# Performance work log

Measured on AMD Instinct MI355X. Metric: run time of the kernel, lower is better.

Reference implementation:

```python
import jax, jax.numpy as jnp
import numpy as np

D = 1024      # model_dim (input_dim)
H = 2048      # hidden_size_per_expert (hardcoded in module)
E = 8         # num_experts
K = 2         # topk
T = 8192      # tokens (batch after view)


def setup_inputs() -> dict:
    key = jax.random.key(0)
    ks = jax.random.split(key, 6)
    s_in = 1.0 / np.sqrt(D)
    s_h = 1.0 / np.sqrt(H)
    return {
        "x": jax.random.normal(ks[0], (T, D), dtype=jnp.float32),
        "wg": jax.random.normal(ks[1], (D, E), dtype=jnp.float32) * s_in,   # gate Linear(D,E,bias=False)
        "w1": jax.random.normal(ks[2], (E, D, H), dtype=jnp.float32) * s_in,
        "b1": jnp.zeros((E, H), dtype=jnp.float32),
        "w2": jax.random.normal(ks[3], (E, H, D), dtype=jnp.float32) * s_h,
        "b2": jnp.zeros((E, D), dtype=jnp.float32),
    }


def _moe(x, wg, w1, b1, w2, b2):
    # top-k gating (Tutel 'top' gate, k=K)
    logits = x @ wg                         # [T,E]
    scores = jax.nn.softmax(logits, -1)     # [T,E]
    topv, topi = jax.lax.top_k(scores, K)   # [T,K]
    sel = jax.nn.one_hot(topi, E, dtype=x.dtype)          # [T,K,E]
    combine = jnp.einsum('tk,tke->te', topv, sel)          # sparse combine weights [T,E]
    # GShard-style load-balance aux loss (top-1 dispatch mask)
    ce = sel[:, 0, :].mean(0)               # fraction of tokens whose top1 is e
    me = scores.mean(0)                     # mean gate prob per expert
    l_aux = jnp.sum(me * ce) * E
    # expert FFN (dense over experts; combine zeros out non-selected)
    h = jax.nn.relu(jnp.einsum('td,edh->teh', x, w1) + b1)  # [T,E,H]
    y = jnp.einsum('teh,ehd->ted', h, w2) + b2              # [T,E,D]
    out = jnp.einsum('te,ted->td', combine, y)              # [T,D]
    return out, l_aux


def reference(x, wg, w1, b1, w2, b2):
    return _moe(x, wg, w1, b1, w2, b2)
```

## Files before the change

### kernel.cpp

```cpp
#include <hip/hip_runtime.h>
#include <stdint.h>

#define T_TOK 8192
#define DIM   1024
#define HID   2048
#define NE    8

#define BM 128
#define BN 128
#define BK 64

#define GB_TOK 32

typedef float floatx4 __attribute__((ext_vector_type(4)));
typedef short shortx8 __attribute__((ext_vector_type(8)));

typedef __attribute__((address_space(3))) void       lds_void;
typedef const __attribute__((address_space(1))) void gbl_void;

__device__ __forceinline__ unsigned short f2bf(float f) {
  unsigned int u = __float_as_uint(f);
  unsigned int r = 0x7fffu + ((u >> 16) & 1u);
  return (unsigned short)((u + r) >> 16);
}

__global__ __launch_bounds__(256) void cast_x_kernel(const float* __restrict__ x,
                                                     unsigned short* __restrict__ xb) {
  size_t i = ((size_t)blockIdx.x * 256 + threadIdx.x) * 4;
  float4 v = *reinterpret_cast<const float4*>(x + i);
  ushort4 o;
  o.x = f2bf(v.x); o.y = f2bf(v.y); o.z = f2bf(v.z); o.w = f2bf(v.w);
  *reinterpret_cast<ushort4*>(xb + i) = o;
}

__global__ __launch_bounds__(256) void transpose_cast_kernel(const float* __restrict__ in,
                                                             unsigned short* __restrict__ out,
                                                             int R, int C) {
  __shared__ float tile[32][33];
  const size_t eoff = (size_t)blockIdx.z * R * C;
  const float* ip = in + eoff;
  unsigned short* op = out + eoff;
  int c0 = blockIdx.x * 32, r0 = blockIdx.y * 32;
  int tx = threadIdx.x, ty = threadIdx.y;
#pragma unroll
  for (int i = 0; i < 4; i++)
    tile[ty + i * 8][tx] = ip[(size_t)(r0 + ty + i * 8) * C + (c0 + tx)];
  __syncthreads();
#pragma unroll
  for (int i = 0; i < 4; i++)
    op[(size_t)(c0 + ty + i * 8) * R + (r0 + tx)] = f2bf(tile[tx][ty + i * 8]);
}

__global__ __launch_bounds__(256) void gate_kernel(const float* __restrict__ x,
                                                   const float* __restrict__ wg,
                                                   int* counts, int* top1cnt, float* ssum,
                                                   int* tok_list, float* wgt_list) {
  __shared__ int   lds_cnt[8];
  __shared__ int   lds_top1[8];
  __shared__ float lds_ssum[4][8];
  __shared__ int   tk_e[GB_TOK][2];
  __shared__ int   tk_r[GB_TOK][2];
  __shared__ float tk_w[GB_TOK][2];
  __shared__ int   base[8];

  const int tid = threadIdx.x;
  const int wave = tid >> 6;
  const int lane = tid & 63;

  if (tid < 8) { lds_cnt[tid] = 0; lds_top1[tid] = 0; }
  if (tid < 32) lds_ssum[tid >> 3][tid & 7] = 0.f;
  __syncthreads();

  float ssum_local[8];
#pragma unroll
  for (int e = 0; e < 8; e++) ssum_local[e] = 0.f;

  for (int it = 0; it < GB_TOK / 4; it++) {
    const int lt = it * 4 + wave;
    const int t = blockIdx.x * GB_TOK + lt;

    float acc[8];
#pragma unroll
    for (int e = 0; e < 8; e++) acc[e] = 0.f;
    const float* xr = x + (size_t)t * DIM;
#pragma unroll
    for (int i = 0; i < 16; i++) {
      int d = i * 64 + lane;
      float xv = xr[d];
      const float4* wr = reinterpret_cast<const float4*>(wg + d * 8);
      float4 w0 = wr[0], w1 = wr[1];
      acc[0] += xv * w0.x; acc[1] += xv * w0.y; acc[2] += xv * w0.z; acc[3] += xv * w0.w;
      acc[4] += xv * w1.x; acc[5] += xv * w1.y; acc[6] += xv * w1.z; acc[7] += xv * w1.w;
    }
#pragma unroll
    for (int e = 0; e < 8; e++) {
#pragma unroll
      for (int off = 32; off > 0; off >>= 1) acc[e] += __shfl_xor(acc[e], off, 64);
    }
    if (lane == 0) {
      float mx = acc[0];
#pragma unroll
      for (int e = 1; e < 8; e++) mx = fmaxf(mx, acc[e]);
      float s[8], sum = 0.f;
#pragma unroll
      for (int e = 0; e < 8; e++) { s[e] = expf(acc[e] - mx); sum += s[e]; }
      float inv = 1.f / sum;
#pragma unroll
      for (int e = 0; e < 8; e++) { s[e] *= inv; ssum_local[e] += s[e]; }
      int i1 = 0;
#pragma unroll
      for (int e = 1; e < 8; e++) if (s[e] > s[i1]) i1 = e;
      int i2 = (i1 == 0) ? 1 : 0;
#pragma unroll
      for (int e = 0; e < 8; e++) if (e != i1 && s[e] > s[i2]) i2 = e;
      atomicAdd(&lds_top1[i1], 1);
      int r1 = atomicAdd(&lds_cnt[i1], 1);
      int r2 = atomicAdd(&lds_cnt[i2], 1);
      tk_e[lt][0] = i1; tk_r[lt][0] = r1; tk_w[lt][0] = s[i1];
      tk_e[lt][1] = i2; tk_r[lt][1] = r2; tk_w[lt][1] = s[i2];
    }
  }
  if (lane == 0) {
#pragma unroll
    for (int e = 0; e < 8; e++) lds_ssum[wave][e] = ssum_local[e];
  }
  __syncthreads();
  if (tid < 8) {
    base[tid] = atomicAdd(&counts[tid], lds_cnt[tid]);
    atomicAdd(&top1cnt[tid], lds_top1[tid]);
    atomicAdd(&ssum[tid],
              lds_ssum[0][tid] + lds_ssum[1][tid] + lds_ssum[2][tid] + lds_ssum[3][tid]);
  }
  __syncthreads();
  if (tid < GB_TOK * 2) {
    int lt = tid >> 1, k = tid & 1;
    int e = tk_e[lt][k];
    int pos = base[e] + tk_r[lt][k];
    tok_list[e * T_TOK + pos] = blockIdx.x * GB_TOK + lt;
    wgt_list[e * T_TOK + pos] = tk_w[lt][k];
  }
}

__global__ void scan_kernel(const int* counts, const int* top1cnt, const float* ssum,
                            int* h_off, float* laux_out) {
  if (threadIdx.x == 0 && blockIdx.x == 0) {
    int off = 0;
    float l = 0.f;
    for (int e = 0; e < 8; e++) {
      h_off[e] = off;
      off += counts[e];
      l += (ssum[e] / (float)T_TOK) * ((float)top1cnt[e] / (float)T_TOK);
    }
    *laux_out = l * (float)NE;
  }
}

template <int MODE>
__global__ __launch_bounds__(256, 4) void moe_gemm_kernel(
    const unsigned short* __restrict__ A_src, const unsigned short* __restrict__ B_src,
    const float* __restrict__ bias, const int* __restrict__ counts,
    const int* __restrict__ h_off, const int* __restrict__ tok_list,
    const float* __restrict__ wgt_list, unsigned short* __restrict__ h_out,
    float* __restrict__ out, int N, int K) {
  __shared__ unsigned short s_a[BM][BK];
  __shared__ unsigned short s_b[BN][BK];

  const int e = blockIdx.z;
  const int n_e = counts[e];
  const int m0 = blockIdx.y * BM;
  if (m0 >= n_e) return;
  const int n0 = blockIdx.x * BN;
  const int tid = threadIdx.x;

  const int lane = tid & 63;
  const int wv = tid >> 6;
  const int lrow = lane >> 3;
  const int lchk = (lane & 7) ^ lrow;

  const unsigned short* a_g[4];
  const unsigned short* b_g[4];
  lds_void* a_l[4];
  lds_void* b_l[4];
#pragma unroll
  for (int c = 0; c < 4; c++) {
    int ra = wv * 32 + c * 8 + lrow;
    int gr = m0 + ra;
    int safe = (gr < n_e) ? gr : (n_e - 1);
    const unsigned short* abase;
    if (MODE == 0) {
      int tok = tok_list[e * T_TOK + safe];
      abase = A_src + (size_t)tok * K;
    } else {
      abase = A_src + (size_t)(h_off[e] + safe) * K;
    }
    a_g[c] = abase + lchk * 8;
    b_g[c] = B_src + ((size_t)e * N + n0 + ra) * K + lchk * 8;
    a_l[c] = (lds_void*)&s_a[wv * 32 + c * 8][0];
    b_l[c] = (lds_void*)&s_b[wv * 32 + c * 8][0];
  }

  const int lm = lane & 15;
  const int quad = lane >> 4;
  const int r7 = lm & 7;
  const int wm = (wv >> 1) * 64;
  const int wn = (wv & 1) * 64;

  floatx4 acc[4][4];
#pragma unroll
  for (int mi = 0; mi < 4; mi++)
#pragma unroll
    for (int ni = 0; ni < 4; ni++) acc[mi][ni] = (floatx4){0.f, 0.f, 0.f, 0.f};

  for (int kt = 0; kt < K; kt += BK) {
#pragma unroll
    for (int c = 0; c < 4; c++) {
      __builtin_amdgcn_global_load_lds((gbl_void*)(a_g[c] + kt), a_l[c], 16, 0, 0);
      __builtin_amdgcn_global_load_lds((gbl_void*)(b_g[c] + kt), b_l[c], 16, 0, 0);
    }
    __syncthreads();
#pragma unroll
    for (int kk = 0; kk < 2; kk++) {
      const int pc = ((kk << 2) + quad) ^ r7;
      shortx8 af[4], bfr[4];
#pragma unroll
      for (int mi = 0; mi < 4; mi++)
        af[mi] = *reinterpret_cast<const shortx8*>(&s_a[wm + mi * 16 + lm][pc << 3]);
#pragma unroll
      for (int ni = 0; ni < 4; ni++)
        bfr[ni] = *reinterpret_cast<const shortx8*>(&s_b[wn + ni * 16 + lm][pc << 3]);
#pragma unroll
      for (int mi = 0; mi < 4; mi++)
#pragma unroll
        for (int ni = 0; ni < 4; ni++)
          acc[mi][ni] = __builtin_amdgcn_mfma_f32_16x16x32_bf16(af[mi], bfr[ni], acc[mi][ni], 0, 0, 0);
    }
    __syncthreads();
  }

#pragma unroll
  for (int mi = 0; mi < 4; mi++) {
#pragma unroll
    for (int r = 0; r < 4; r++) {
      int row = m0 + wm + mi * 16 + quad * 4 + r;
      if (row >= n_e) continue;
      if (MODE == 0) {
        size_t base = (size_t)(h_off[e] + row) * N;
#pragma unroll
        for (int ni = 0; ni < 4; ni++) {
          int col = n0 + wn + ni * 16 + lm;
          float v = acc[mi][ni][r] + bias[e * N + col];
          v = fmaxf(v, 0.f);
          h_out[base + col] = f2bf(v);
        }
      } else {
        int tok = tok_list[e * T_TOK + row];
        float wgt = wgt_list[e * T_TOK + row];
        size_t base = (size_t)tok * N;
#pragma unroll
        for (int ni = 0; ni < 4; ni++) {
          int col = n0 + wn + ni * 16 + lm;
          float v = wgt * (acc[mi][ni][r] + bias[e * N + col]);
          atomicAdd(&out[base + col], v);
        }
      }
    }
  }
}

extern "C" void kernel_launch(void* const* d_in, const int* in_sizes, int n_in,
                              void* d_out, int out_size, void* d_ws, size_t ws_size,
                              hipStream_t stream) {
  const float* x  = (const float*)d_in[0];
  const float* wg = (const float*)d_in[1];
  const float* w1 = (const float*)d_in[2];
  const float* b1 = (const float*)d_in[3];
  const float* w2 = (const float*)d_in[4];
  const float* b2 = (const float*)d_in[5];
  float* out = (float*)d_out;

  char* ws = (char*)d_ws;
  int*            counts   = (int*)(ws + 0);
  int*            top1cnt  = (int*)(ws + 32);
  float*          ssum     = (float*)(ws + 64);
  int*            h_off    = (int*)(ws + 96);
  int*            tok_list = (int*)(ws + 256);
  float*          wgt_list = (float*)(ws + 262400);
  unsigned short* x_bf     = (unsigned short*)(ws + 524544);
  unsigned short* w1t      = (unsigned short*)(ws + 17301760);
  unsigned short* w2t      = (unsigned short*)(ws + 50856192);
  unsigned short* h_buf    = (unsigned short*)(ws + 84410624);

  hipMemsetAsync(ws, 0, 256, stream);
  hipMemsetAsync(d_out, 0, (size_t)out_size * sizeof(float), stream);

  cast_x_kernel<<<(T_TOK * DIM) / 1024, 256, 0, stream>>>(x, x_bf);

  dim3 tb(32, 8);
  transpose_cast_kernel<<<dim3(HID / 32, DIM / 32, NE), tb, 0, stream>>>(w1, w1t, DIM, HID);
  transpose_cast_kernel<<<dim3(DIM / 32, HID / 32, NE), tb, 0, stream>>>(w2, w2t, HID, DIM);

  gate_kernel<<<T_TOK / GB_TOK, 256, 0, stream>>>(x, wg, counts, top1cnt, ssum, tok_list, wgt_list);
  scan_kernel<<<1, 64, 0, stream>>>(counts, top1cnt, ssum, h_off, out + (size_t)T_TOK * DIM);

  moe_gemm_kernel<0><<<dim3(HID / BN, T_TOK / BM, NE), 256, 0, stream>>>(
      x_bf, w1t, b1, counts, h_off, tok_list, wgt_list, h_buf, nullptr, HID, DIM);
  moe_gemm_kernel<1><<<dim3(DIM / BN, T_TOK / BM, NE), 256, 0, stream>>>(
      h_buf, w2t, b2, counts, h_off, tok_list, wgt_list, nullptr, out, DIM, HID);
}
```

Baseline: 486.3 us.

## Use 256x256 double-buffered GEMM tiles and fuse x bf16 cast into gate

The grouped expert GEMMs move from 128x128 tiles with 256 threads to 256x256 tiles with 512 threads (8 waves, each owning a 128x64 sub-tile). The LDS buffers are double-buffered so the next K-slice is fetched while the current one feeds the MFMAs, which removes one barrier per K-step and improves operand reuse. Separately, the bf16 cast of x now happens inside the gate kernel, which already reads x, so one kernel launch and one full read of x go away. The larger tiles use 128 KB of LDS per block and more accumulator registers, and produce fewer blocks and more padding waste on experts with uneven token counts.

```diff
diff --git a/kernel.cpp b/kernel.cpp
--- a/kernel.cpp
+++ b/kernel.cpp
@@ -6,8 +6,8 @@
 #define HID   2048
 #define NE    8
 
-#define BM 128
-#define BN 128
+#define BM 256
+#define BN 256
 #define BK 64
 
 #define GB_TOK 32
@@ -22,15 +22,6 @@
   unsigned int u = __float_as_uint(f);
   unsigned int r = 0x7fffu + ((u >> 16) & 1u);
   return (unsigned short)((u + r) >> 16);
-}
-
-__global__ __launch_bounds__(256) void cast_x_kernel(const float* __restrict__ x,
-                                                     unsigned short* __restrict__ xb) {
-  size_t i = ((size_t)blockIdx.x * 256 + threadIdx.x) * 4;
-  float4 v = *reinterpret_cast<const float4*>(x + i);
-  ushort4 o;
-  o.x = f2bf(v.x); o.y = f2bf(v.y); o.z = f2bf(v.z); o.w = f2bf(v.w);
-  *reinterpret_cast<ushort4*>(xb + i) = o;
 }
 
 __global__ __launch_bounds__(256) void transpose_cast_kernel(const float* __restrict__ in,
@@ -53,6 +44,7 @@
 
 __global__ __launch_bounds__(256) void gate_kernel(const float* __restrict__ x,
                                                    const float* __restrict__ wg,
+                                                   unsigned short* __restrict__ xb,
                                                    int* counts, int* top1cnt, float* ssum,
                                                    int* tok_list, float* wgt_list) {
   __shared__ int   lds_cnt[8];
@@ -83,10 +75,12 @@
 #pragma unroll
     for (int e = 0; e < 8; e++) acc[e] = 0.f;
     const float* xr = x + (size_t)t * DIM;
+    unsigned short* xw = xb + (size_t)t * DIM;
 #pragma unroll
     for (int i = 0; i < 16; i++) {
       int d = i * 64 + lane;
       float xv = xr[d];
+      xw[d] = f2bf(xv);
       const float4* wr = reinterpret_cast<const float4*>(wg + d * 8);
       float4 w0 = wr[0], w1 = wr[1];
       acc[0] += xv * w0.x; acc[1] += xv * w0.y; acc[2] += xv * w0.z; acc[3] += xv * w0.w;
@@ -156,14 +150,14 @@
 }
 
 template <int MODE>
-__global__ __launch_bounds__(256, 4) void moe_gemm_kernel(
+__global__ __launch_bounds__(512, 2) void moe_gemm_kernel(
     const unsigned short* __restrict__ A_src, const unsigned short* __restrict__ B_src,
     const float* __restrict__ bias, const int* __restrict__ counts,
     const int* __restrict__ h_off, const int* __restrict__ tok_list,
     const float* __restrict__ wgt_list, unsigned short* __restrict__ h_out,
     float* __restrict__ out, int N, int K) {
-  __shared__ unsigned short s_a[BM][BK];
-  __shared__ unsigned short s_b[BN][BK];
+  __shared__ unsigned short s_a[2][BM][BK];
+  __shared__ unsigned short s_b[2][BN][BK];
 
   const int e = blockIdx.z;
   const int n_e = counts[e];
@@ -179,11 +173,9 @@
 
   const unsigned short* a_g[4];
   const unsigned short* b_g[4];
-  lds_void* a_l[4];
-  lds_void* b_l[4];
 #pragma unroll
   for (int c = 0; c < 4; c++) {
-    int ra = wv * 32 + c * 8 + lrow;
+    int ra = c * 64 + wv * 8 + lrow;
     int gr = m0 + ra;
     int safe = (gr < n_e) ? gr : (n_e - 1);
     const unsigned short* abase;
@@ -195,50 +187,59 @@
     }
     a_g[c] = abase + lchk * 8;
     b_g[c] = B_src + ((size_t)e * N + n0 + ra) * K + lchk * 8;
-    a_l[c] = (lds_void*)&s_a[wv * 32 + c * 8][0];
-    b_l[c] = (lds_void*)&s_b[wv * 32 + c * 8][0];
-  }
+  }
+
+  auto STAGE = [&](int buf, int kt) {
+#pragma unroll
+    for (int c = 0; c < 4; c++) {
+      __builtin_amdgcn_global_load_lds((gbl_void*)(a_g[c] + kt),
+                                       (lds_void*)&s_a[buf][c * 64 + wv * 8][0], 16, 0, 0);
+      __builtin_amdgcn_global_load_lds((gbl_void*)(b_g[c] + kt),
+                                       (lds_void*)&s_b[buf][c * 64 + wv * 8][0], 16, 0, 0);
+    }
+  };
 
   const int lm = lane & 15;
   const int quad = lane >> 4;
   const int r7 = lm & 7;
-  const int wm = (wv >> 1) * 64;
-  const int wn = (wv & 1) * 64;
-
-  floatx4 acc[4][4];
-#pragma unroll
-  for (int mi = 0; mi < 4; mi++)
+  const int wm = (wv >> 2) * 128;
+  const int wn = (wv & 3) * 64;
+
+  floatx4 acc[8][4];
+#pragma unroll
+  for (int mi = 0; mi < 8; mi++)
 #pragma unroll
     for (int ni = 0; ni < 4; ni++) acc[mi][ni] = (floatx4){0.f, 0.f, 0.f, 0.f};
 
-  for (int kt = 0; kt < K; kt += BK) {
-#pragma unroll
-    for (int c = 0; c < 4; c++) {
-      __builtin_amdgcn_global_load_lds((gbl_void*)(a_g[c] + kt), a_l[c], 16, 0, 0);
-      __builtin_amdgcn_global_load_lds((gbl_void*)(b_g[c] + kt), b_l[c], 16, 0, 0);
-    }
-    __syncthreads();
+  const int NT = K / BK;
+  STAGE(0, 0);
+  __syncthreads();
+
+  int cur = 0;
+  for (int t = 0; t < NT; ++t) {
+    if (t + 1 < NT) STAGE(cur ^ 1, (t + 1) * BK);
 #pragma unroll
     for (int kk = 0; kk < 2; kk++) {
       const int pc = ((kk << 2) + quad) ^ r7;
-      shortx8 af[4], bfr[4];
-#pragma unroll
-      for (int mi = 0; mi < 4; mi++)
-        af[mi] = *reinterpret_cast<const shortx8*>(&s_a[wm + mi * 16 + lm][pc << 3]);
+      shortx8 af[8], bfr[4];
+#pragma unroll
+      for (int mi = 0; mi < 8; mi++)
+        af[mi] = *reinterpret_cast<const shortx8*>(&s_a[cur][wm + mi * 16 + lm][pc << 3]);
 #pragma unroll
       for (int ni = 0; ni < 4; ni++)
-        bfr[ni] = *reinterpret_cast<const shortx8*>(&s_b[wn + ni * 16 + lm][pc << 3]);
-#pragma unroll
-      for (int mi = 0; mi < 4; mi++)
+        bfr[ni] = *reinterpret_cast<const shortx8*>(&s_b[cur][wn + ni * 16 + lm][pc << 3]);
+#pragma unroll
+      for (int mi = 0; mi < 8; mi++)
 #pragma unroll
         for (int ni = 0; ni < 4; ni++)
           acc[mi][ni] = __builtin_amdgcn_mfma_f32_16x16x32_bf16(af[mi], bfr[ni], acc[mi][ni], 0, 0, 0);
     }
     __syncthreads();
-  }
-
-#pragma unroll
-  for (int mi = 0; mi < 4; mi++) {
+    cur ^= 1;
+  }
+
+#pragma unroll
+  for (int mi = 0; mi < 8; mi++) {
 #pragma unroll
     for (int r = 0; r < 4; r++) {
       int row = m0 + wm + mi * 16 + quad * 4 + r;
@@ -293,17 +294,16 @@
   hipMemsetAsync(ws, 0, 256, stream);
   hipMemsetAsync(d_out, 0, (size_t)out_size * sizeof(float), stream);
 
-  cast_x_kernel<<<(T_TOK * DIM) / 1024, 256, 0, stream>>>(x, x_bf);
-
   dim3 tb(32, 8);
   transpose_cast_kernel<<<dim3(HID / 32, DIM / 32, NE), tb, 0, stream>>>(w1, w1t, DIM, HID);
   transpose_cast_kernel<<<dim3(DIM / 32, HID / 32, NE), tb, 0, stream>>>(w2, w2t, HID, DIM);
 
-  gate_kernel<<<T_TOK / GB_TOK, 256, 0, stream>>>(x, wg, counts, top1cnt, ssum, tok_list, wgt_list);
+  gate_kernel<<<T_TOK / GB_TOK, 256, 0, stream>>>(x, wg, x_bf, counts, top1cnt, ssum,
+                                                  tok_list, wgt_list);
   scan_kernel<<<1, 64, 0, stream>>>(counts, top1cnt, ssum, h_off, out + (size_t)T_TOK * DIM);
 
-  moe_gemm_kernel<0><<<dim3(HID / BN, T_TOK / BM, NE), 256, 0, stream>>>(
+  moe_gemm_kernel<0><<<dim3(HID / BN, T_TOK / BM, NE), 512, 0, stream>>>(
       x_bf, w1t, b1, counts, h_off, tok_list, wgt_list, h_buf, nullptr, HID, DIM);
-  moe_gemm_kernel<1><<<dim3(DIM / BN, T_TOK / BM, NE), 256, 0, stream>>>(
+  moe_gemm_kernel<1><<<dim3(DIM / BN, T_TOK / BM, NE), 512, 0, stream>>>(
       h_buf, w2t, b2, counts, h_off, tok_list, wgt_list, nullptr, out, DIM, HID);
 }
```

After: 574.0 us. 18.0% more time.
